# Kernel optimization log

Measured on AMD Instinct MI355X. Metric: run time of the kernel, lower is better.

The kernel has to match this reference:

```python
import jax, jax.numpy as jnp
import numpy as np

HEAD_DIM = 128
N_HEADS = 16
N_KV_HEADS = 4
CHUNK = 256
TOPK = 4
ROPE_THETA = 10000.0


def apply_rope(x, pos):
    # x: [B, S, H, D], NeoX-style (half-split) rotary as in flash-attn RotaryEmbedding
    d = x.shape[-1]
    inv_freq = 1.0 / (ROPE_THETA ** (jnp.arange(0, d, 2, dtype=jnp.float32) / d))  # [D/2]
    ang = pos.astype(jnp.float32)[:, None] * inv_freq[None, :]  # [S, D/2]
    cos = jnp.cos(ang)[None, :, None, :]
    sin = jnp.sin(ang)[None, :, None, :]
    x1, x2 = x[..., : d // 2], x[..., d // 2:]
    return jnp.concatenate([x1 * cos - x2 * sin, x2 * cos + x1 * sin], axis=-1)


def setup_inputs() -> dict:
    key = jax.random.key(0)
    ks = jax.random.split(key, 5)
    B, S, H = 2, 2048, 2048
    hidden_states = jax.random.normal(ks[0], (B, S, H), dtype=jnp.float32)
    wq = jax.random.normal(ks[1], (H, N_HEADS * HEAD_DIM), dtype=jnp.float32) * 0.02
    wk = jax.random.normal(ks[2], (H, N_KV_HEADS * HEAD_DIM), dtype=jnp.float32) * 0.02
    wv = jax.random.normal(ks[3], (H, N_KV_HEADS * HEAD_DIM), dtype=jnp.float32) * 0.02
    wo = jax.random.normal(ks[4], (N_HEADS * HEAD_DIM, H), dtype=jnp.float32) * 0.02
    return {"hidden_states": hidden_states, "wq": wq, "wk": wk, "wv": wv, "wo": wo}


def reference(hidden_states, wq, wk, wv, wo):
    B, S, _ = hidden_states.shape
    q = (hidden_states @ wq).reshape(B, S, N_HEADS, HEAD_DIM)
    k = (hidden_states @ wk).reshape(B, S, N_KV_HEADS, HEAD_DIM)
    v = (hidden_states @ wv).reshape(B, S, N_KV_HEADS, HEAD_DIM)

    pos = jnp.arange(S)
    q = apply_rope(q, pos)
    k = apply_rope(k, pos)

    # GQA: repeat_interleave kv heads to match query heads
    g = N_HEADS // N_KV_HEADS
    k = jnp.repeat(k, g, axis=2)  # [B,S,H,D]
    v = jnp.repeat(v, g, axis=2)

    # ---- MoBA gating: q . mean(K_chunk) ----
    N = S // CHUNK  # number of chunks
    kmean = k.reshape(B, N, CHUNK, N_HEADS, HEAD_DIM).mean(axis=2)  # [B,N,H,D]
    gate = jnp.einsum('bnhd,bshd->bhsn', kmean, q)  # [B,H,S,N]

    chunk_ids = jnp.arange(N)
    chunk_end = (chunk_ids + 1) * CHUNK
    q_chunk = pos // CHUNK
    # chunks not fully before the query are not gate candidates
    gate = jnp.where(pos[None, None, :, None] >= chunk_end[None, None, None, :], gate, -jnp.inf)
    # query's own chunk is always selected
    gate = jnp.where(q_chunk[None, None, :, None] == chunk_ids[None, None, None, :], jnp.inf, gate)

    _, idx = jax.lax.top_k(gate, min(TOPK, N))  # [B,H,S,K]
    sel = jnp.any(idx[..., None] == chunk_ids, axis=-2)  # [B,H,S,N] bool

    # expand chunk selection to per-key mask; combine with causal mask
    allowed = sel[:, :, :, pos // CHUNK]  # [B,H,S,S]
    causal = pos[:, None] >= pos[None, :]  # [S,S]
    mask = allowed & causal[None, None]

    scale = HEAD_DIM ** -0.5
    scores = jnp.einsum('bshd,bthd->bhst', q, k) * scale
    scores = jnp.where(mask, scores, -jnp.inf)
    probs = jax.nn.softmax(scores, axis=-1)
    o = jnp.einsum('bhst,bthd->bshd', probs, v).reshape(B, S, N_HEADS * HEAD_DIM)
    return o @ wo
```

## Files before the change

### kernel.cpp

```cpp
#include <hip/hip_runtime.h>
#include <stdint.h>
#include <math.h>

typedef _Float16 f16x8 __attribute__((ext_vector_type(8)));
typedef float    f32x4 __attribute__((ext_vector_type(4)));
typedef __attribute__((address_space(1))) void as1_void;
typedef __attribute__((address_space(3))) void as3_void;

__device__ __forceinline__ unsigned short f2h(float x) {
    _Float16 h = (_Float16)x;
    return __builtin_bit_cast(unsigned short, h);
}
__device__ __forceinline__ float h2f(unsigned short u) {
    return (float)__builtin_bit_cast(_Float16, u);
}
__device__ __forceinline__ void glds16(const void* g, void* l) {
    __builtin_amdgcn_global_load_lds((as1_void*)g, (as3_void*)l, 16, 0, 0);
}

#define DPPF(v, ctrl) __builtin_bit_cast(float, \
    __builtin_amdgcn_update_dpp(0, __builtin_bit_cast(int, (v)), (ctrl), 0xF, 0xF, true))


#define TAU 0.015
#define FLAGCAP 4096

__global__ void setup_kernel(float* __restrict__ ct, float* __restrict__ st,
                             double* __restrict__ km, int* __restrict__ flagcnt) {
    int gid = blockIdx.x * 256 + threadIdx.x;
    if (gid < 16) flagcnt[gid] = 0;
    if (gid < 8192) km[gid] = 0.0;
    int i = gid & 63, s = gid >> 6;
    float xf = (float)i * (1.0f / 64.0f);
    float pf = (float)pow(10000.0, (double)xf);
    float inv = 1.0f / pf;
    float ang = (float)s * inv;
    ct[gid] = (float)cos((double)ang);
    st[gid] = (float)sin((double)ang);
}

__global__ __launch_bounds__(256)
void ksum_kernel(const float* __restrict__ hs, const float* __restrict__ ct,
                 const float* __restrict__ st, double* __restrict__ Act,
                 double* __restrict__ Ast) {
    __shared__ float Hs[16][68];
    __shared__ float Tc[16][68];
    __shared__ float Ts[16][68];
    int bn = blockIdx.y;
    int h0 = blockIdx.x * 64;
    int b = bn >> 3, n = bn & 7;
    int t = threadIdx.x;
    int tx = t & 15, ty = t >> 4;
    int d0 = tx * 4, hl0 = ty * 4;
    int si = t & 15, g4 = (t >> 4) * 4;
    double ac[4][4] = {}, as_[4][4] = {};
    for (int s0 = 0; s0 < 256; s0 += 16) {
        __syncthreads();
        int srow = n * 256 + s0 + si;
        *(float4*)&Hs[si][g4] = *(const float4*)&hs[(size_t)(b * 2048 + srow) * 2048 + h0 + g4];
        *(float4*)&Tc[si][g4] = *(const float4*)&ct[srow * 64 + g4];
        *(float4*)&Ts[si][g4] = *(const float4*)&st[srow * 64 + g4];
        __syncthreads();
        #pragma unroll
        for (int kk = 0; kk < 16; ++kk) {
            double hv[4], cv[4], sv[4];
            #pragma unroll
            for (int j = 0; j < 4; ++j) hv[j] = (double)Hs[kk][hl0 + j];
            #pragma unroll
            for (int i = 0; i < 4; ++i) { cv[i] = (double)Tc[kk][d0 + i]; sv[i] = (double)Ts[kk][d0 + i]; }
            #pragma unroll
            for (int i = 0; i < 4; ++i)
                #pragma unroll
                for (int j = 0; j < 4; ++j) {
                    ac[i][j]  = fma(cv[i], hv[j], ac[i][j]);
                    as_[i][j] = fma(sv[i], hv[j], as_[i][j]);
                }
        }
    }
    #pragma unroll
    for (int j = 0; j < 4; ++j) {
        size_t rb = ((size_t)bn * 2048 + h0 + hl0 + j) * 64 + d0;
        double2 c0 = {ac[0][j], ac[1][j]},  c1 = {ac[2][j], ac[3][j]};
        double2 s0_ = {as_[0][j], as_[1][j]}, s1_ = {as_[2][j], as_[3][j]};
        *(double2*)&Act[rb] = c0; *(double2*)&Act[rb + 2] = c1;
        *(double2*)&Ast[rb] = s0_; *(double2*)&Ast[rb + 2] = s1_;
    }
}

__global__ __launch_bounds__(256)
void kmeanw_kernel(const double* __restrict__ Act, const double* __restrict__ Ast,
                   const float* __restrict__ wk, double* __restrict__ km) {
    __shared__ double red[256];
    int blk = blockIdx.x;
    int hp = blk & 31, kvh = (blk >> 5) & 3, bn = blk >> 7;
    int t = threadIdx.x;
    int d = t & 127, sub = t >> 7;
    int jj = d & 63;
    int col1 = kvh * 128 + d;
    int col2 = kvh * 128 + (d ^ 64);
    double sgn = (d < 64) ? -1.0 : 1.0;
    const double* actb = Act + (size_t)bn * 2048 * 64;
    const double* astb = Ast + (size_t)bn * 2048 * 64;
    double a1 = 0.0, a2 = 0.0, b1 = 0.0, b2 = 0.0;
    double c1 = 0.0, c2 = 0.0, d1 = 0.0, d2 = 0.0;
    int hbeg = hp * 64 + sub * 32;
    #pragma unroll 2
    for (int h = hbeg; h < hbeg + 32; h += 4) {
        a1 = fma(actb[(size_t)(h + 0) * 64 + jj], (double)wk[(size_t)(h + 0) * 512 + col1], a1);
        a2 = fma(astb[(size_t)(h + 0) * 64 + jj], (double)wk[(size_t)(h + 0) * 512 + col2], a2);
        b1 = fma(actb[(size_t)(h + 1) * 64 + jj], (double)wk[(size_t)(h + 1) * 512 + col1], b1);
        b2 = fma(astb[(size_t)(h + 1) * 64 + jj], (double)wk[(size_t)(h + 1) * 512 + col2], b2);
        c1 = fma(actb[(size_t)(h + 2) * 64 + jj], (double)wk[(size_t)(h + 2) * 512 + col1], c1);
        c2 = fma(astb[(size_t)(h + 2) * 64 + jj], (double)wk[(size_t)(h + 2) * 512 + col2], c2);
        d1 = fma(actb[(size_t)(h + 3) * 64 + jj], (double)wk[(size_t)(h + 3) * 512 + col1], d1);
        d2 = fma(astb[(size_t)(h + 3) * 64 + jj], (double)wk[(size_t)(h + 3) * 512 + col2], d2);
    }
    double acc1 = (a1 + b1) + (c1 + d1);
    double acc2 = (a2 + b2) + (c2 + d2);
    red[t] = acc1 + sgn * acc2;
    __syncthreads();
    if (t < 128) {
        double v = red[t] + red[t + 128];
        atomicAdd(&km[((size_t)bn * 4 + kvh) * 128 + d], v * (1.0 / 256.0));
    }
}

__global__ __launch_bounds__(256)
void ropegate_kernel(float* __restrict__ C, const float* __restrict__ ct,
                     const float* __restrict__ st, const double* __restrict__ km,
                     unsigned int* __restrict__ maskbuf,
                     int* __restrict__ flagcnt, int* __restrict__ flaglist) {
    __shared__ float qbuf[2048];
    int bs = blockIdx.x;
    int s = bs & 2047, b = bs >> 11;
    int t = threadIdx.x;
    size_t base = (size_t)bs * 3072;
    #pragma unroll
    for (int it = 0; it < 5; ++it) {
        int p = t + it * 256;
        int hd = p >> 6, i = p & 63;
        float cs = ct[s * 64 + i], sn = st[s * 64 + i];
        float x1 = C[base + hd * 128 + i];
        float x2 = C[base + hd * 128 + i + 64];
        float n1 = x1 * cs - x2 * sn;
        float n2 = x2 * cs + x1 * sn;
        C[base + hd * 128 + i] = n1;
        C[base + hd * 128 + i + 64] = n2;
        if (hd < 16) { qbuf[hd * 128 + i] = n1; qbuf[hd * 128 + i + 64] = n2; }
    }
    __syncthreads();
    int wave = t >> 6, lane = t & 63;
    int qc = s >> 8;
    const double INF = __builtin_inf();
    #pragma unroll
    for (int ii = 0; ii < 4; ++ii) {
        int h = wave * 4 + ii;
        int kvh = h >> 2;
        double q0 = (double)qbuf[h * 128 + lane];
        double q1 = (double)qbuf[h * 128 + 64 + lane];
        double g[8];
        #pragma unroll
        for (int n = 0; n < 8; ++n) {
            size_t kb = (size_t)((b * 8 + n) * 4 + kvh) * 128;
            double v = q0 * km[kb + lane] + q1 * km[kb + 64 + lane];
            #pragma unroll
            for (int off = 32; off; off >>= 1) v += __shfl_xor(v, off);
            g[n] = v;
        }
        #pragma unroll
        for (int n = 0; n < 8; ++n) {
            if (n == qc)                g[n] = INF;
            else if (s < (n + 1) * 256) g[n] = -INF;
        }
        unsigned int msk = 0;
        for (int p = 0; p < 4; ++p) {
            double best = -INF; int bi = -1;
            #pragma unroll
            for (int n = 0; n < 8; ++n)
                if (!((msk >> n) & 1) && g[n] > best) { best = g[n]; bi = n; }
            if (bi >= 0) msk |= 1u << bi;
        }
        if (lane == 0) {
            int wid = ((b * 16 + h) << 11) + s;
            maskbuf[wid] = msk;
            if (qc >= 4) {
                double worst_in = INF, best_out = -INF;
                #pragma unroll
                for (int n = 0; n < 8; ++n) {
                    if ((msk >> n) & 1) worst_in = fmin(worst_in, g[n]);
                    else if (g[n] > -1e300) best_out = fmax(best_out, g[n]);
                }
                if (worst_in - best_out < TAU) {
                    int ix = atomicAdd(&flagcnt[h], 1);
                    if (ix < FLAGCAP) flaglist[h * FLAGCAP + ix] = wid;
                }
            }
        }
    }
}

__global__ __launch_bounds__(256)
void repair_kernel(const float* __restrict__ hs, const float* __restrict__ wq,
                   const float* __restrict__ ct, const float* __restrict__ st,
                   const double* __restrict__ km, const int* __restrict__ flagcnt,
                   const int* __restrict__ flaglist, unsigned int* __restrict__ maskbuf) {
    __shared__ double hrow_d[2048];
    __shared__ double red[8][132];
    __shared__ double qs[128];
    int hb = blockIdx.x >> 8;
    int nflag = flagcnt[hb];
    if (nflag > FLAGCAP) nflag = FLAGCAP;
    const int* list = flaglist + hb * FLAGCAP;
    int t = threadIdx.x;
    int dg = t & 31, sub = t >> 5;
    for (int idx = blockIdx.x & 255; idx < nflag; idx += 256) {
        int wid = list[idx];
        int s = wid & 2047;
        int h = (wid >> 11) & 15;
        int b = wid >> 15;
        int kvh = h >> 2;
        __syncthreads();
        {
            const float4* src = (const float4*)(hs + (size_t)(b * 2048 + s) * 2048);
            float4 v0 = src[t], v1 = src[t + 256];
            hrow_d[4 * t + 0] = (double)v0.x; hrow_d[4 * t + 1] = (double)v0.y;
            hrow_d[4 * t + 2] = (double)v0.z; hrow_d[4 * t + 3] = (double)v0.w;
            hrow_d[4 * t + 1024 + 0] = (double)v1.x; hrow_d[4 * t + 1024 + 1] = (double)v1.y;
            hrow_d[4 * t + 1024 + 2] = (double)v1.z; hrow_d[4 * t + 1024 + 3] = (double)v1.w;
        }
        __syncthreads();
        const float* wbase = wq + (size_t)(sub * 256) * 2048 + h * 128 + dg * 4;
        const double* hb_ = hrow_d + sub * 256;
        double a0 = 0, a1 = 0, a2 = 0, a3 = 0;
        double c0 = 0, c1 = 0, c2 = 0, c3 = 0;
        #pragma unroll 4
        for (int k = 0; k < 256; k += 2) {
            float4 w0 = *(const float4*)&wbase[(size_t)k * 2048];
            float4 w1 = *(const float4*)&wbase[(size_t)(k + 1) * 2048];
            double h0 = hb_[k], h1 = hb_[k + 1];
            a0 = fma(h0, (double)w0.x, a0); a1 = fma(h0, (double)w0.y, a1);
            a2 = fma(h0, (double)w0.z, a2); a3 = fma(h0, (double)w0.w, a3);
            c0 = fma(h1, (double)w1.x, c0); c1 = fma(h1, (double)w1.y, c1);
            c2 = fma(h1, (double)w1.z, c2); c3 = fma(h1, (double)w1.w, c3);
        }
        red[sub][dg * 4 + 0] = a0 + c0; red[sub][dg * 4 + 1] = a1 + c1;
        red[sub][dg * 4 + 2] = a2 + c2; red[sub][dg * 4 + 3] = a3 + c3;
        __syncthreads();
        if (t < 128) {
            double v = 0.0;
            #pragma unroll
            for (int u = 0; u < 8; ++u) v += red[u][t];
            qs[t] = v;
        }
        __syncthreads();
        if (t < 64) {
            double c  = (double)ct[s * 64 + t];
            double sn = (double)st[s * 64 + t];
            double x1 = qs[t], x2 = qs[t + 64];
            qs[t]      = x1 * c - x2 * sn;
            qs[t + 64] = x2 * c + x1 * sn;
        }
        __syncthreads();
        if (t < 64) {
            double g[8];
            #pragma unroll
            for (int n = 0; n < 8; ++n) {
                size_t kb = (size_t)((b * 8 + n) * 4 + kvh) * 128;
                double v = qs[t] * km[kb + t] + qs[t + 64] * km[kb + 64 + t];
                #pragma unroll
                for (int off = 32; off; off >>= 1) v += __shfl_xor(v, off);
                g[n] = v;
            }
            int qc = s >> 8;
            const double INF = __builtin_inf();
            #pragma unroll
            for (int n = 0; n < 8; ++n) {
                if (n == qc)                g[n] = INF;
                else if (s < (n + 1) * 256) g[n] = -INF;
            }
            unsigned int msk = 0;
            for (int p = 0; p < 4; ++p) {
                double best = -INF; int bi = -1;
                #pragma unroll
                for (int n = 0; n < 8; ++n)
                    if (!((msk >> n) & 1) && g[n] > best) { best = g[n]; bi = n; }
                if (bi >= 0) msk |= 1u << bi;
            }
            if (t == 0) maskbuf[wid] = msk;
        }
        __syncthreads();
    }
}


__global__ void split_kernel(const float* __restrict__ src,
                             unsigned short* __restrict__ hi, int n4) {
    int i = blockIdx.x * 256 + threadIdx.x;
    if (i >= n4) return;
    float4 v = ((const float4*)src)[i];
    ushort4 h;
    h.x = f2h(v.x); h.y = f2h(v.y); h.z = f2h(v.z); h.w = f2h(v.w);
    ((ushort4*)hi)[i] = h;
}

__global__ void packall_kernel(const float* __restrict__ wq, const float* __restrict__ wk,
                               const float* __restrict__ wv, const float* __restrict__ wo,
                               unsigned short* __restrict__ Wh, unsigned short* __restrict__ Woh) {
    int gid = blockIdx.x * 256 + threadIdx.x;
    if (gid < 3072 * 512) {
        int n  = gid % 3072;
        int kg = gid / 3072;
        const float* src; int ldn, col;
        if (n < 2048)      { src = wq; ldn = 2048; col = n; }
        else if (n < 2560) { src = wk; ldn = 512;  col = n - 2048; }
        else               { src = wv; ldn = 512;  col = n - 2560; }
        int k0 = kg * 4;
        ushort4 h;
        h.x = f2h(src[(size_t)(k0 + 0) * ldn + col]);
        h.y = f2h(src[(size_t)(k0 + 1) * ldn + col]);
        h.z = f2h(src[(size_t)(k0 + 2) * ldn + col]);
        h.w = f2h(src[(size_t)(k0 + 3) * ldn + col]);
        *(ushort4*)&Wh[(size_t)n * 2048 + k0] = h;
    } else {
        int g2 = gid - 3072 * 512;
        int n  = g2 % 2048;
        int kg = g2 / 2048;
        int k0 = kg * 4;
        ushort4 h;
        h.x = f2h(wo[(size_t)(k0 + 0) * 2048 + n]);
        h.y = f2h(wo[(size_t)(k0 + 1) * 2048 + n]);
        h.z = f2h(wo[(size_t)(k0 + 2) * 2048 + n]);
        h.w = f2h(wo[(size_t)(k0 + 3) * 2048 + n]);
        *(ushort4*)&Woh[(size_t)n * 2048 + k0] = h;
    }
}

__global__ __launch_bounds__(256, 2)
void gemm_kernel(const unsigned short* __restrict__ A_g, const unsigned short* __restrict__ B_g,
                 float* __restrict__ Cg, int M, int N, int K) {
    __shared__ unsigned short Ah[128 * 32];
    __shared__ unsigned short Bh[128 * 32];
    int n0 = blockIdx.x * 128, m0 = blockIdx.y * 128;
    int t = threadIdx.x;
    int wave = t >> 6, lane = t & 63;
    int quad = lane >> 4, l15 = lane & 15;
    int wm = (wave >> 1) * 64, wn = (wave & 1) * 64;

    f32x4 acc[4][4];
    f32x4 zero = {0.f, 0.f, 0.f, 0.f};
    for (int i = 0; i < 4; ++i)
        for (int j = 0; j < 4; ++j) acc[i][j] = zero;

    int srow = lane >> 2, scol = (lane & 3) * 8;
    const unsigned short* Ag0 = &A_g[(size_t)(m0 + wave * 16 + srow) * K + scol];
    const unsigned short* Ag1 = &A_g[(size_t)(m0 + 64 + wave * 16 + srow) * K + scol];
    const unsigned short* Bg0 = &B_g[(size_t)(n0 + wave * 16 + srow) * K + scol];
    const unsigned short* Bg1 = &B_g[(size_t)(n0 + 64 + wave * 16 + srow) * K + scol];
    unsigned short* Al0 = &Ah[(wave * 16) * 32];
    unsigned short* Al1 = &Ah[(64 + wave * 16) * 32];
    unsigned short* Bl0 = &Bh[(wave * 16) * 32];
    unsigned short* Bl1 = &Bh[(64 + wave * 16) * 32];

    for (int k0 = 0; k0 < K; k0 += 32) {
        __syncthreads();
        glds16(Ag0 + k0, Al0);
        glds16(Ag1 + k0, Al1);
        glds16(Bg0 + k0, Bl0);
        glds16(Bg1 + k0, Bl1);
        __syncthreads();
        f16x8 ah[4], bh[4];
        #pragma unroll
        for (int i = 0; i < 4; ++i) {
            ah[i] = *(const f16x8*)&Ah[(wm + i * 16 + l15) * 32 + quad * 8];
            bh[i] = *(const f16x8*)&Bh[(wn + i * 16 + l15) * 32 + quad * 8];
        }
        #pragma unroll
        for (int i = 0; i < 4; ++i)
            #pragma unroll
            for (int j = 0; j < 4; ++j)
                acc[i][j] = __builtin_amdgcn_mfma_f32_16x16x32_f16(ah[i], bh[j], acc[i][j], 0, 0, 0);
    }
    #pragma unroll
    for (int i = 0; i < 4; ++i)
        #pragma unroll
        for (int j = 0; j < 4; ++j)
            #pragma unroll
            for (int r = 0; r < 4; ++r) {
                int row = m0 + wm + i * 16 + quad * 4 + r;
                int col = n0 + wn + j * 16 + l15;
                Cg[(size_t)row * N + col] = acc[i][j][r];
            }
}

__global__ void kvprep_kernel(const float* __restrict__ C, unsigned short* __restrict__ Kh,
                              unsigned short* __restrict__ Vt) {
    __shared__ unsigned short vt[128][72];
    int blk = blockIdx.x;
    int kt = blk & 31, kvh = (blk >> 5) & 3, b = blk >> 7;
    int t = threadIdx.x;
    int key0 = kt * 64;
    #pragma unroll
    for (int it = 0; it < 8; ++it) {
        int idx = t + it * 256;
        int r = idx >> 5, c = (idx & 31) * 4;
        size_t rowb = (size_t)(b * 2048 + key0 + r) * 3072;
        float4 kv = *(const float4*)&C[rowb + 2048 + kvh * 128 + c];
        ushort4 u; u.x = f2h(kv.x); u.y = f2h(kv.y); u.z = f2h(kv.z); u.w = f2h(kv.w);
        *(ushort4*)&Kh[((size_t)(b * 4 + kvh) * 2048 + key0 + r) * 128 + c] = u;
        float4 vv = *(const float4*)&C[rowb + 2560 + kvh * 128 + c];
        vt[c + 0][r] = f2h(vv.x); vt[c + 1][r] = f2h(vv.y);
        vt[c + 2][r] = f2h(vv.z); vt[c + 3][r] = f2h(vv.w);
    }
    __syncthreads();
    #pragma unroll
    for (int it = 0; it < 8; ++it) {
        int idx = t + it * 256;
        int d = idx >> 4, c4 = (idx & 15) * 4;
        *(ushort4*)&Vt[((size_t)(b * 4 + kvh) * 128 + d) * 2048 + key0 + c4] =
            *(ushort4*)&vt[d][c4];
    }
}

__global__ __launch_bounds__(256, 3)
void attn_kernel(const float* __restrict__ C, const unsigned short* __restrict__ Kh,
                 const unsigned short* __restrict__ Vt,
                 const unsigned int* __restrict__ maskbuf,
                 unsigned short* __restrict__ Og) {
    __shared__ unsigned short qv[8704];
    __shared__ unsigned short k_s[8448];
    __shared__ unsigned short p_s[4352];
    __shared__ int kb_list[32];
    __shared__ int nsub_s;
    __shared__ unsigned int umask;

    int bid = blockIdx.x;
    int qt = 31 - (bid >> 5);
    int bh = bid & 31;
    int h = bh & 15, b = bh >> 4;
    int t = threadIdx.x;
    int wave = t >> 6, lane = t & 63;
    int quad = lane >> 4, l15 = lane & 15;
    int w16 = wave * 16;
    int q0 = qt * 64, qc = q0 >> 8, kvh = h >> 2;
    const float NEGINF = -__builtin_inff();

    #pragma unroll
    for (int it = 0; it < 8; ++it) {
        int idx = t + it * 256;
        int r = idx >> 5, c = (idx & 31) * 4;
        float4 v4 = *(const float4*)&C[(size_t)(b * 2048 + q0 + r) * 3072 + h * 128 + c];
        ushort4 u; u.x = f2h(v4.x); u.y = f2h(v4.y); u.z = f2h(v4.z); u.w = f2h(v4.w);
        *(ushort4*)&qv[r * 132 + c] = u;
    }
    if (t == 0) umask = 0;
    int mbase = ((b * 16 + h) << 11) + q0;
    unsigned int am[4];
    #pragma unroll
    for (int r = 0; r < 4; ++r)
        am[r] = maskbuf[mbase + w16 + quad * 4 + r];
    __syncthreads();
    if (t < 64) atomicOr(&umask, maskbuf[mbase + t]);
    f16x8 aq[4];
    #pragma unroll
    for (int ks = 0; ks < 4; ++ks)
        aq[ks] = *(const f16x8*)&qv[(w16 + l15) * 132 + ks * 32 + quad * 8];
    __syncthreads();
    if (t == 0) {
        unsigned int um = umask;
        int n = 0;
        for (int c = 0; c <= qc; ++c) {
            if (!((um >> c) & 1)) continue;
            int submax = (c == qc) ? ((q0 & 255) >> 6) : 3;
            for (int sub = 0; sub <= submax; ++sub) kb_list[n++] = c * 256 + sub * 64;
        }
        nsub_s = n;
    }
    __syncthreads();
    int nsub = nsub_s;

    float m_i[4], l_i[4];
    f32x4 o_acc[8];
    #pragma unroll
    for (int r = 0; r < 4; ++r) { m_i[r] = NEGINF; l_i[r] = 0.f; }
    #pragma unroll
    for (int n = 0; n < 8; ++n) o_acc[n] = (f32x4){0.f, 0.f, 0.f, 0.f};
    const float scale = 0.08838834764831845f;
    const unsigned short* Kb = Kh + (size_t)(b * 4 + kvh) * 2048 * 128;
    const unsigned short* Vb = Vt + (size_t)(b * 4 + kvh) * 128 * 2048;

    int kr = t >> 5, kc = (t & 31) * 4;
    int vr = t >> 4, vc = (t & 15) * 4;

    ushort4 kpre[8], vpre[8];
    {
        int kb0 = kb_list[0];
        #pragma unroll
        for (int it = 0; it < 8; ++it) {
            kpre[it] = *(const ushort4*)&Kb[(size_t)(kb0 + kr + it * 8) * 128 + kc];
            vpre[it] = *(const ushort4*)&Vb[(size_t)(vr + it * 16) * 2048 + kb0 + vc];
        }
    }

    for (int i = 0; i < nsub; ++i) {
        int kbase = kb_list[i];
        __syncthreads();
        #pragma unroll
        for (int it = 0; it < 8; ++it) {
            *(ushort4*)&k_s[(kr + it * 8) * 132 + kc] = kpre[it];
            *(ushort4*)&qv[(vr + it * 16) * 68 + vc] = vpre[it];
        }
        __syncthreads();
        if (i + 1 < nsub) {
            int kbn = kb_list[i + 1];
            #pragma unroll
            for (int it = 0; it < 8; ++it) {
                kpre[it] = *(const ushort4*)&Kb[(size_t)(kbn + kr + it * 8) * 128 + kc];
                vpre[it] = *(const ushort4*)&Vb[(size_t)(vr + it * 16) * 2048 + kbn + vc];
            }
        }
        f32x4 s[4];
        #pragma unroll
        for (int j = 0; j < 4; ++j) {
            f32x4 sj = {0.f, 0.f, 0.f, 0.f};
            #pragma unroll
            for (int ks = 0; ks < 4; ++ks) {
                f16x8 bf = *(const f16x8*)&k_s[(j * 16 + l15) * 132 + ks * 32 + quad * 8];
                sj = __builtin_amdgcn_mfma_f32_16x16x32_f16(aq[ks], bf, sj, 0, 0, 0);
            }
            s[j] = sj;
        }
        #pragma unroll
        for (int r = 0; r < 4; ++r) {
            int qpos = q0 + w16 + quad * 4 + r;
            bool allow = (am[r] >> (kbase >> 8)) & 1;
            float sv[4], rmax = NEGINF;
            #pragma unroll
            for (int j = 0; j < 4; ++j) {
                int kpos = kbase + j * 16 + l15;
                float x = s[j][r] * scale;
                if (!allow || kpos > qpos) x = NEGINF;
                sv[j] = x;
                rmax = fmaxf(rmax, x);
            }
            rmax = fmaxf(rmax, DPPF(rmax, 0xB1));
            rmax = fmaxf(rmax, DPPF(rmax, 0x4E));
            rmax = fmaxf(rmax, DPPF(rmax, 0x141));
            rmax = fmaxf(rmax, DPPF(rmax, 0x128));
            float mnew = fmaxf(m_i[r], rmax);
            float alpha = (m_i[r] == NEGINF) ? 0.f : __expf(m_i[r] - mnew);
            float ps[4], lsum = 0.f;
            #pragma unroll
            for (int j = 0; j < 4; ++j) {
                float p = (sv[j] == NEGINF) ? 0.f : __expf(sv[j] - mnew);
                ps[j] = p; lsum += p;
            }
            lsum += DPPF(lsum, 0xB1);
            lsum += DPPF(lsum, 0x4E);
            lsum += DPPF(lsum, 0x141);
            lsum += DPPF(lsum, 0x128);
            l_i[r] = l_i[r] * alpha + lsum;
            m_i[r] = mnew;
            #pragma unroll
            for (int n = 0; n < 8; ++n) o_acc[n][r] *= alpha;
            #pragma unroll
            for (int j = 0; j < 4; ++j)
                p_s[(w16 + quad * 4 + r) * 68 + j * 16 + l15] = f2h(ps[j]);
        }
        f16x8 pa0 = *(const f16x8*)&p_s[(w16 + l15) * 68 + quad * 8];
        f16x8 pa1 = *(const f16x8*)&p_s[(w16 + l15) * 68 + 32 + quad * 8];
        #pragma unroll
        for (int n = 0; n < 8; ++n) {
            f16x8 b0 = *(const f16x8*)&qv[(n * 16 + l15) * 68 + quad * 8];
            f16x8 b1 = *(const f16x8*)&qv[(n * 16 + l15) * 68 + 32 + quad * 8];
            o_acc[n] = __builtin_amdgcn_mfma_f32_16x16x32_f16(pa0, b0, o_acc[n], 0, 0, 0);
            o_acc[n] = __builtin_amdgcn_mfma_f32_16x16x32_f16(pa1, b1, o_acc[n], 0, 0, 0);
        }
    }
    __syncthreads();
    #pragma unroll
    for (int r = 0; r < 4; ++r) {
        float inv = (l_i[r] > 0.f) ? 1.f / l_i[r] : 0.f;
        #pragma unroll
        for (int n = 0; n < 8; ++n)
            k_s[(w16 + quad * 4 + r) * 132 + n * 16 + l15] = f2h(o_acc[n][r] * inv);
    }
    __syncthreads();
    #pragma unroll
    for (int it = 0; it < 8; ++it) {
        int idx = t + it * 256;
        int r = idx >> 5, cpos = (idx & 31) * 4;
        *(ushort4*)&Og[(size_t)(b * 2048 + q0 + r) * 2048 + h * 128 + cpos] =
            *(ushort4*)&k_s[r * 132 + cpos];
    }
}

extern "C" void kernel_launch(void* const* d_in, const int* in_sizes, int n_in,
                              void* d_out, int out_size, void* d_ws, size_t ws_size,
                              hipStream_t stream) {
    const float* hs = (const float*)d_in[0];
    const float* wq = (const float*)d_in[1];
    const float* wk = (const float*)d_in[2];
    const float* wv = (const float*)d_in[3];
    const float* wo = (const float*)d_in[4];
    float* out = (float*)d_out;
    char* ws = (char*)d_ws;

    double*         Act  = (double*)       (ws + 37748736);
    double*         Ast  = (double*)       (ws + 54525952);
    unsigned short* hsh  = (unsigned short*)(ws + 0);
    unsigned short* Wth  = (unsigned short*)(ws + 16777216);
    unsigned short* woth = (unsigned short*)(ws + 29360128);
    float*          Cqkv = (float*)        (ws + 37748736);
    unsigned short* Og   = (unsigned short*)(ws + 88080384);
    double*         km64 = (double*)       (ws + 104857600);
    unsigned int*   mskb = (unsigned int*) (ws + 104923136);
    float*          ct   = (float*)        (ws + 105447424);
    float*          st   = (float*)        (ws + 105971712);
    unsigned short* Kh   = (unsigned short*)(ws + 106496000);
    unsigned short* Vt   = (unsigned short*)(ws + 114884608);
    int*            fcnt = (int*)          (ws + 123273216);
    int*            flst = (int*)          (ws + 123273280);

    setup_kernel  <<<512, 256, 0, stream>>>(ct, st, km64, fcnt);
    ksum_kernel   <<<dim3(32, 16), 256, 0, stream>>>(hs, ct, st, Act, Ast);
    kmeanw_kernel <<<2048, 256, 0, stream>>>(Act, Ast, wk, km64);
    split_kernel  <<<8192, 256, 0, stream>>>(hs, hsh, 2097152);
    packall_kernel<<<10240, 256, 0, stream>>>(wq, wk, wv, wo, Wth, woth);
    gemm_kernel   <<<dim3(24, 32), 256, 0, stream>>>(hsh, Wth, Cqkv, 4096, 3072, 2048);
    ropegate_kernel<<<4096, 256, 0, stream>>>(Cqkv, ct, st, km64, mskb, fcnt, flst);
    repair_kernel <<<4096, 256, 0, stream>>>(hs, wq, ct, st, km64, fcnt, flst, mskb);
    kvprep_kernel <<<256, 256, 0, stream>>>(Cqkv, Kh, Vt);
    attn_kernel   <<<1024, 256, 0, stream>>>(Cqkv, Kh, Vt, mskb, Og);
    gemm_kernel   <<<dim3(16, 32), 256, 0, stream>>>(Og, woth, out, 4096, 2048, 2048);
}
```

Measured before the change: 578.8 us.

## Double attention query tile to 128 rows per block to reuse K/V tiles

```diff
diff --git a/kernel.cpp b/kernel.cpp
--- a/kernel.cpp
+++ b/kernel.cpp
@@ -421,56 +421,59 @@
     }
 }
 
-__global__ __launch_bounds__(256, 3)
+__global__ __launch_bounds__(256, 2)
 void attn_kernel(const float* __restrict__ C, const unsigned short* __restrict__ Kh,
                  const unsigned short* __restrict__ Vt,
                  const unsigned int* __restrict__ maskbuf,
                  unsigned short* __restrict__ Og) {
-    __shared__ unsigned short qv[8704];
-    __shared__ unsigned short k_s[8448];
-    __shared__ unsigned short p_s[4352];
+    __shared__ unsigned short SH[34048];
     __shared__ int kb_list[32];
     __shared__ int nsub_s;
     __shared__ unsigned int umask;
+    const int KOFF = 16896, POFF = 25344;
 
     int bid = blockIdx.x;
-    int qt = 31 - (bid >> 5);
+    int qt = 15 - (bid >> 5);
     int bh = bid & 31;
     int h = bh & 15, b = bh >> 4;
     int t = threadIdx.x;
     int wave = t >> 6, lane = t & 63;
     int quad = lane >> 4, l15 = lane & 15;
-    int w16 = wave * 16;
-    int q0 = qt * 64, qc = q0 >> 8, kvh = h >> 2;
+    int w32 = wave * 32;
+    int q0 = qt * 128, qc = q0 >> 8, kvh = h >> 2;
     const float NEGINF = -__builtin_inff();
 
     #pragma unroll
-    for (int it = 0; it < 8; ++it) {
+    for (int it = 0; it < 16; ++it) {
         int idx = t + it * 256;
         int r = idx >> 5, c = (idx & 31) * 4;
         float4 v4 = *(const float4*)&C[(size_t)(b * 2048 + q0 + r) * 3072 + h * 128 + c];
         ushort4 u; u.x = f2h(v4.x); u.y = f2h(v4.y); u.z = f2h(v4.z); u.w = f2h(v4.w);
-        *(ushort4*)&qv[r * 132 + c] = u;
+        *(ushort4*)&SH[r * 132 + c] = u;
     }
     if (t == 0) umask = 0;
     int mbase = ((b * 16 + h) << 11) + q0;
-    unsigned int am[4];
-    #pragma unroll
-    for (int r = 0; r < 4; ++r)
-        am[r] = maskbuf[mbase + w16 + quad * 4 + r];
-    __syncthreads();
-    if (t < 64) atomicOr(&umask, maskbuf[mbase + t]);
-    f16x8 aq[4];
-    #pragma unroll
-    for (int ks = 0; ks < 4; ++ks)
-        aq[ks] = *(const f16x8*)&qv[(w16 + l15) * 132 + ks * 32 + quad * 8];
+    unsigned int am[2][4];
+    #pragma unroll
+    for (int rg = 0; rg < 2; ++rg)
+        #pragma unroll
+        for (int r = 0; r < 4; ++r)
+            am[rg][r] = maskbuf[mbase + w32 + rg * 16 + quad * 4 + r];
+    __syncthreads();
+    if (t < 128) atomicOr(&umask, maskbuf[mbase + t]);
+    f16x8 aq[2][4];
+    #pragma unroll
+    for (int rg = 0; rg < 2; ++rg)
+        #pragma unroll
+        for (int ks = 0; ks < 4; ++ks)
+            aq[rg][ks] = *(const f16x8*)&SH[(w32 + rg * 16 + l15) * 132 + ks * 32 + quad * 8];
     __syncthreads();
     if (t == 0) {
         unsigned int um = umask;
         int n = 0;
         for (int c = 0; c <= qc; ++c) {
             if (!((um >> c) & 1)) continue;
-            int submax = (c == qc) ? ((q0 & 255) >> 6) : 3;
+            int submax = (c == qc) ? (((q0 & 255) >> 6) + 1) : 3;
             for (int sub = 0; sub <= submax; ++sub) kb_list[n++] = c * 256 + sub * 64;
         }
         nsub_s = n;
@@ -478,12 +481,15 @@
     __syncthreads();
     int nsub = nsub_s;
 
-    float m_i[4], l_i[4];
-    f32x4 o_acc[8];
-    #pragma unroll
-    for (int r = 0; r < 4; ++r) { m_i[r] = NEGINF; l_i[r] = 0.f; }
-    #pragma unroll
-    for (int n = 0; n < 8; ++n) o_acc[n] = (f32x4){0.f, 0.f, 0.f, 0.f};
+    float m_i[2][4], l_i[2][4];
+    f32x4 o_acc[2][8];
+    #pragma unroll
+    for (int rg = 0; rg < 2; ++rg) {
+        #pragma unroll
+        for (int r = 0; r < 4; ++r) { m_i[rg][r] = NEGINF; l_i[rg][r] = 0.f; }
+        #pragma unroll
+        for (int n = 0; n < 8; ++n) o_acc[rg][n] = (f32x4){0.f, 0.f, 0.f, 0.f};
+    }
     const float scale = 0.08838834764831845f;
     const unsigned short* Kb = Kh + (size_t)(b * 4 + kvh) * 2048 * 128;
     const unsigned short* Vb = Vt + (size_t)(b * 4 + kvh) * 128 * 2048;
@@ -506,8 +512,8 @@
         __syncthreads();
         #pragma unroll
         for (int it = 0; it < 8; ++it) {
-            *(ushort4*)&k_s[(kr + it * 8) * 132 + kc] = kpre[it];
-            *(ushort4*)&qv[(vr + it * 16) * 68 + vc] = vpre[it];
+            *(ushort4*)&SH[KOFF + (kr + it * 8) * 132 + kc] = kpre[it];
+            *(ushort4*)&SH[(vr + it * 16) * 68 + vc] = vpre[it];
         }
         __syncthreads();
         if (i + 1 < nsub) {
@@ -518,79 +524,92 @@
                 vpre[it] = *(const ushort4*)&Vb[(size_t)(vr + it * 16) * 2048 + kbn + vc];
             }
         }
-        f32x4 s[4];
+        f32x4 s[2][4];
         #pragma unroll
         for (int j = 0; j < 4; ++j) {
-            f32x4 sj = {0.f, 0.f, 0.f, 0.f};
+            f32x4 s0 = {0.f, 0.f, 0.f, 0.f}, s1 = {0.f, 0.f, 0.f, 0.f};
             #pragma unroll
             for (int ks = 0; ks < 4; ++ks) {
-                f16x8 bf = *(const f16x8*)&k_s[(j * 16 + l15) * 132 + ks * 32 + quad * 8];
-                sj = __builtin_amdgcn_mfma_f32_16x16x32_f16(aq[ks], bf, sj, 0, 0, 0);
-            }
-            s[j] = sj;
-        }
+                f16x8 bf = *(const f16x8*)&SH[KOFF + (j * 16 + l15) * 132 + ks * 32 + quad * 8];
+                s0 = __builtin_amdgcn_mfma_f32_16x16x32_f16(aq[0][ks], bf, s0, 0, 0, 0);
+                s1 = __builtin_amdgcn_mfma_f32_16x16x32_f16(aq[1][ks], bf, s1, 0, 0, 0);
+            }
+            s[0][j] = s0; s[1][j] = s1;
+        }
+        #pragma unroll
+        for (int rg = 0; rg < 2; ++rg) {
+            #pragma unroll
+            for (int r = 0; r < 4; ++r) {
+                int qpos = q0 + w32 + rg * 16 + quad * 4 + r;
+                bool allow = (am[rg][r] >> (kbase >> 8)) & 1;
+                float sv[4], rmax = NEGINF;
+                #pragma unroll
+                for (int j = 0; j < 4; ++j) {
+                    int kpos = kbase + j * 16 + l15;
+                    float x = s[rg][j][r] * scale;
+                    if (!allow || kpos > qpos) x = NEGINF;
+                    sv[j] = x;
+                    rmax = fmaxf(rmax, x);
+                }
+                rmax = fmaxf(rmax, DPPF(rmax, 0xB1));
+                rmax = fmaxf(rmax, DPPF(rmax, 0x4E));
+                rmax = fmaxf(rmax, DPPF(rmax, 0x141));
+                rmax = fmaxf(rmax, DPPF(rmax, 0x128));
+                float mnew = fmaxf(m_i[rg][r], rmax);
+                float alpha = (m_i[rg][r] == NEGINF) ? 0.f : __expf(m_i[rg][r] - mnew);
+                float ps[4], lsum = 0.f;
+                #pragma unroll
+                for (int j = 0; j < 4; ++j) {
+                    float p = (sv[j] == NEGINF) ? 0.f : __expf(sv[j] - mnew);
+                    ps[j] = p; lsum += p;
+                }
+                lsum += DPPF(lsum, 0xB1);
+                lsum += DPPF(lsum, 0x4E);
+                lsum += DPPF(lsum, 0x141);
+                lsum += DPPF(lsum, 0x128);
+                l_i[rg][r] = l_i[rg][r] * alpha + lsum;
+                m_i[rg][r] = mnew;
+                #pragma unroll
+                for (int n = 0; n < 8; ++n) o_acc[rg][n][r] *= alpha;
+                #pragma unroll
+                for (int j = 0; j < 4; ++j)
+                    SH[POFF + (w32 + rg * 16 + quad * 4 + r) * 68 + j * 16 + l15] = f2h(ps[j]);
+            }
+        }
+        f16x8 pa[2][2];
+        #pragma unroll
+        for (int rg = 0; rg < 2; ++rg) {
+            pa[rg][0] = *(const f16x8*)&SH[POFF + (w32 + rg * 16 + l15) * 68 + quad * 8];
+            pa[rg][1] = *(const f16x8*)&SH[POFF + (w32 + rg * 16 + l15) * 68 + 32 + quad * 8];
+        }
+        #pragma unroll
+        for (int n = 0; n < 8; ++n) {
+            f16x8 b0 = *(const f16x8*)&SH[(n * 16 + l15) * 68 + quad * 8];
+            f16x8 b1 = *(const f16x8*)&SH[(n * 16 + l15) * 68 + 32 + quad * 8];
+            o_acc[0][n] = __builtin_amdgcn_mfma_f32_16x16x32_f16(pa[0][0], b0, o_acc[0][n], 0, 0, 0);
+            o_acc[0][n] = __builtin_amdgcn_mfma_f32_16x16x32_f16(pa[0][1], b1, o_acc[0][n], 0, 0, 0);
+            o_acc[1][n] = __builtin_amdgcn_mfma_f32_16x16x32_f16(pa[1][0], b0, o_acc[1][n], 0, 0, 0);
+            o_acc[1][n] = __builtin_amdgcn_mfma_f32_16x16x32_f16(pa[1][1], b1, o_acc[1][n], 0, 0, 0);
+        }
+    }
+    __syncthreads();
+    #pragma unroll
+    for (int rg = 0; rg < 2; ++rg)
         #pragma unroll
         for (int r = 0; r < 4; ++r) {
-            int qpos = q0 + w16 + quad * 4 + r;
-            bool allow = (am[r] >> (kbase >> 8)) & 1;
-            float sv[4], rmax = NEGINF;
-            #pragma unroll
-            for (int j = 0; j < 4; ++j) {
-                int kpos = kbase + j * 16 + l15;
-                float x = s[j][r] * scale;
-                if (!allow || kpos > qpos) x = NEGINF;
-                sv[j] = x;
-                rmax = fmaxf(rmax, x);
-            }
-            rmax = fmaxf(rmax, DPPF(rmax, 0xB1));
-            rmax = fmaxf(rmax, DPPF(rmax, 0x4E));
-            rmax = fmaxf(rmax, DPPF(rmax, 0x141));
-            rmax = fmaxf(rmax, DPPF(rmax, 0x128));
-            float mnew = fmaxf(m_i[r], rmax);
-            float alpha = (m_i[r] == NEGINF) ? 0.f : __expf(m_i[r] - mnew);
-            float ps[4], lsum = 0.f;
-            #pragma unroll
-            for (int j = 0; j < 4; ++j) {
-                float p = (sv[j] == NEGINF) ? 0.f : __expf(sv[j] - mnew);
-                ps[j] = p; lsum += p;
-            }
-            lsum += DPPF(lsum, 0xB1);
-            lsum += DPPF(lsum, 0x4E);
-            lsum += DPPF(lsum, 0x141);
-            lsum += DPPF(lsum, 0x128);
-            l_i[r] = l_i[r] * alpha + lsum;
-            m_i[r] = mnew;
-            #pragma unroll
-            for (int n = 0; n < 8; ++n) o_acc[n][r] *= alpha;
-            #pragma unroll
-            for (int j = 0; j < 4; ++j)
-                p_s[(w16 + quad * 4 + r) * 68 + j * 16 + l15] = f2h(ps[j]);
-        }
-        f16x8 pa0 = *(const f16x8*)&p_s[(w16 + l15) * 68 + quad * 8];
-        f16x8 pa1 = *(const f16x8*)&p_s[(w16 + l15) * 68 + 32 + quad * 8];
-        #pragma unroll
-        for (int n = 0; n < 8; ++n) {
-            f16x8 b0 = *(const f16x8*)&qv[(n * 16 + l15) * 68 + quad * 8];
-            f16x8 b1 = *(const f16x8*)&qv[(n * 16 + l15) * 68 + 32 + quad * 8];
-            o_acc[n] = __builtin_amdgcn_mfma_f32_16x16x32_f16(pa0, b0, o_acc[n], 0, 0, 0);
-            o_acc[n] = __builtin_amdgcn_mfma_f32_16x16x32_f16(pa1, b1, o_acc[n], 0, 0, 0);
-        }
-    }
-    __syncthreads();
-    #pragma unroll
-    for (int r = 0; r < 4; ++r) {
-        float inv = (l_i[r] > 0.f) ? 1.f / l_i[r] : 0.f;
-        #pragma unroll
-        for (int n = 0; n < 8; ++n)
-            k_s[(w16 + quad * 4 + r) * 132 + n * 16 + l15] = f2h(o_acc[n][r] * inv);
-    }
-    __syncthreads();
-    #pragma unroll
-    for (int it = 0; it < 8; ++it) {
+            float inv = (l_i[rg][r] > 0.f) ? 1.f / l_i[rg][r] : 0.f;
+            #pragma unroll
+            for (int n = 0; n < 8; ++n)
+                SH[KOFF + (w32 + rg * 16 + quad * 4 + r) * 128 + n * 16 + l15] =
+                    f2h(o_acc[rg][n][r] * inv);
+        }
+    __syncthreads();
+    #pragma unroll
+    for (int it = 0; it < 16; ++it) {
         int idx = t + it * 256;
-        int r = idx >> 5, cpos = (idx & 31) * 4;
-        *(ushort4*)&Og[(size_t)(b * 2048 + q0 + r) * 2048 + h * 128 + cpos] =
-            *(ushort4*)&k_s[r * 132 + cpos];
+        int r = idx >> 5, c4 = (idx & 31) * 4;
+        *(ushort4*)&Og[(size_t)(b * 2048 + q0 + r) * 2048 + h * 128 + c4] =
+            *(ushort4*)&SH[KOFF + r * 128 + c4];
     }
 }
 
@@ -630,6 +649,6 @@
     ropegate_kernel<<<4096, 256, 0, stream>>>(Cqkv, ct, st, km64, mskb, fcnt, flst);
     repair_kernel <<<4096, 256, 0, stream>>>(hs, wq, ct, st, km64, fcnt, flst, mskb);
     kvprep_kernel <<<256, 256, 0, stream>>>(Cqkv, Kh, Vt);
-    attn_kernel   <<<1024, 256, 0, stream>>>(Cqkv, Kh, Vt, mskb, Og);
+    attn_kernel   <<<512, 256, 0, stream>>>(Cqkv, Kh, Vt, mskb, Og);
     gemm_kernel   <<<dim3(16, 32), 256, 0, stream>>>(Og, woth, out, 4096, 2048, 2048);
 }
```

After: 607.1 us. 4.9% more time.
